# Kernel tuning notes

Hardware: AMD Instinct MI355X
Metric: run time of the kernel (lower is better)

Reference implementation:

```python
import jax, jax.numpy as jnp
import numpy as np
from functools import partial

# --- constants from module init / yolov5 NMS conventions ---
CONF_THRES = 0.25
IOU_THRES = 0.45
PATCH_CONF = 0.001
GN = jnp.array([640.0, 640.0, 640.0, 640.0])  # img_size[[1,0,1,0]]
MAX_WH = 4096.0       # per-class NMS offset trick
K_CLEAN = 256         # fixed-size cap for clean detections (max_det=1000 effectively)
K_PATCH = 1024        # fixed-size cap for patch detections (max_det=30000 effectively)
MAXDET_CLEAN = 1000
MAXDET_PATCH = 30000
B, N, NC = 8, 25200, 80


def xywh2xyxy(x):
    xy, wh = x[..., :2], x[..., 2:4]
    return jnp.concatenate([xy - wh * 0.5, xy + wh * 0.5], axis=-1)


def pairwise_iou(a, b):
    # a: [A,4], b: [B,4] -> [A,B] jaccard overlap (same math as IoU.get_iou)
    tl = jnp.maximum(a[:, None, :2], b[None, :, :2])
    br = jnp.minimum(a[:, None, 2:], b[None, :, 2:])
    wh = jnp.clip(br - tl, 0.0)
    inter = wh[..., 0] * wh[..., 1]
    area_a = (a[:, 2] - a[:, 0]) * (a[:, 3] - a[:, 1])
    area_b = (b[:, 2] - b[:, 0]) * (b[:, 3] - b[:, 1])
    return inter / (area_a[:, None] + area_b[None, :] - inter)


def greedy_nms(iou_mat, valid, iou_thres):
    # iou_mat: [K,K] (score-sorted order), valid: [K] bool. Greedy suppression.
    K = valid.shape[0]
    j = jnp.arange(K)

    def body(i, keep):
        suppress = keep[i] & (iou_mat[i] > iou_thres) & (j > i)
        return keep & ~suppress

    return jax.lax.fori_loop(0, K, body, valid)


def _nms_single(pred, conf_thres, K, max_det):
    # pred: [N, 5+nc] raw yolov5 prediction for one image
    boxes = xywh2xyxy(pred[:, :4])
    obj = pred[:, 4]
    cls_scores = pred[:, 5:] * obj[:, None]          # conf = obj * cls
    conf = cls_scores.max(axis=-1)
    cls = jnp.argmax(cls_scores, axis=-1).astype(pred.dtype)
    valid = (obj > conf_thres) & (conf > conf_thres)
    mscore = jnp.where(valid, conf, -1.0)
    _, idx = jax.lax.top_k(mscore, K)                # fixed-size candidate prefilter
    bk, ck, vk = boxes[idx], cls[idx], valid[idx]
    off_boxes = bk + (ck * MAX_WH)[:, None]          # class-offset NMS
    iou = pairwise_iou(off_boxes, off_boxes)
    keep = greedy_nms(jax.lax.stop_gradient(iou), vk, IOU_THRES)
    keep = keep & (jnp.cumsum(keep.astype(jnp.int32)) <= max_det)
    return bk, ck, keep


def _forward(output_clean, output_patch):
    nms_clean = jax.vmap(lambda p: _nms_single(p, CONF_THRES, K_CLEAN, MAXDET_CLEAN))
    nms_patch = jax.vmap(lambda p: _nms_single(p, PATCH_CONF, K_PATCH, MAXDET_PATCH))
    bc, cc, kc = nms_clean(output_clean)   # [B,Kc,4],[B,Kc],[B,Kc]
    bp, cp, kp = nms_patch(output_patch)   # [B,Kp,4],[B,Kp],[B,Kp]
    bc_n = bc / GN
    bp_n = bp / GN

    def per_img(bp_i, cp_i, kp_i, bc_i, cc_i, kc_i):
        iou = pairwise_iou(bp_i, bc_i)                       # [Kp, Kc]
        match = kp_i[:, None] & (cp_i[:, None] == cc_i[None, :])
        tm = jnp.max(jnp.where(match, iou, 0.0), axis=0)     # max IoU per clean det
        return jnp.sum(jnp.where(kc_i, tm, 0.0)), jnp.sum(kc_i.astype(jnp.float32))

    sums, counts = jax.vmap(per_img)(bp_n, cp, kp, bc_n, cc, kc)
    total, cnt = sums.sum(), counts.sum()
    return jnp.where(cnt > 0, 1.0 - total / jnp.maximum(cnt, 1.0), 1.0)


def setup_inputs() -> dict:
    key = jax.random.key(0)
    k1, k2 = jax.random.split(key)

    def make(k):
        kxy, kwh, ko, kc = jax.random.split(k, 4)
        xy = jax.random.uniform(kxy, (B, N, 2)) * 608.0 + 16.0   # centers in-frame
        wh = jax.random.uniform(kwh, (B, N, 2)) * 96.0 + 8.0     # plausible box sizes
        obj = jax.random.uniform(ko, (B, N, 1))
        cls = jax.random.uniform(kc, (B, N, NC))
        return jnp.concatenate([xy, wh, obj, cls], axis=-1)

    return {"output_clean": make(k1), "output_patch": make(k2)}


def reference(output_clean, output_patch):
    return _forward(output_clean, output_patch)
```

## Files before the change

kernel.cpp:

```cpp
#include <hip/hip_runtime.h>

#define N_ANCH 25200
#define NCLS   80
#define ROW    85
#define NIMG   16
#define KMAX   1024
#define NBINS  1024
#define CAND_CAP 4096
#define SC_ROWS 64
#define SC_CHUNKS 394
#define SC_FLOATS (SC_ROWS*ROW)
#define PCHUNK 64

typedef unsigned long long u64;
typedef unsigned int u32;

#define OFF_KEYS 0ull
#define OFF_HIST 3225600ull
#define OFF_DIAG 3291136ull
#define OFF_SEL  3422208ull
#define OFF_BOX  3553280ull
#define OFF_CLS  3815424ull
#define OFF_RINIT 3880960ull
#define OFF_KEEP 3883008ull
#define WS_NEED  3948544ull
#define ZERO_BYTES 65536ull

#define DMA16(gsrc, ldst) \
    __builtin_amdgcn_global_load_lds( \
        (const __attribute__((address_space(1))) void*)(gsrc), \
        (__attribute__((address_space(3))) void*)(ldst), 16, 0, 0)

__device__ __forceinline__ int key_bin(u64 key) {
    u32 hi = (u32)(key >> 32);
    if (hi == 0u) return 0;
    float conf = __uint_as_float(hi - 0x40000000u);
    int b = 1 + (int)(conf * 1022.0f);
    return b > 1023 ? 1023 : b;
}

__device__ __forceinline__ u64 readlane64(u64 v, int src) {
    u32 lo = (u32)__builtin_amdgcn_readlane((int)(u32)(v & 0xffffffffull), src);
    u32 hi = (u32)__builtin_amdgcn_readlane((int)(u32)(v >> 32), src);
    return ((u64)hi << 32) | (u64)lo;
}

__device__ __forceinline__ u64 shfl64_xor(u64 v, int m) {
    int lo = __shfl_xor((int)(u32)(v & 0xffffffffull), m, 64);
    int hi = __shfl_xor((int)(u32)(v >> 32), m, 64);
    return ((u64)(u32)hi << 32) | (u64)(u32)lo;
}

__global__ __launch_bounds__(128) void k_score(const float* __restrict__ clean,
                                               const float* __restrict__ patch,
                                               u64* __restrict__ keys,
                                               int* __restrict__ hist)
{
    __shared__ float lbuf[SC_FLOATS];
    __shared__ int bh[NBINS];
    const int t = threadIdx.x;
    const int wv = t >> 6, lane = t & 63;
    const int bid = blockIdx.x;
    const int b = bid / SC_CHUNKS;
    const int chunk = bid - b * SC_CHUNKS;
    for (int i = t; i < NBINS; i += 128) bh[i] = 0;
    const float* bufbase = (b < 8) ? clean : patch;
    const float* ibase = bufbase + (size_t)((b < 8) ? b : b - 8) * N_ANCH * ROW;
    const int base = chunk * SC_ROWS;
    const float* g = ibase + (size_t)base * ROW;
    if (chunk != SC_CHUNKS - 1) {
        if (wv == 0) {
            #pragma unroll
            for (int u = 0; u < 11; ++u)
                DMA16(g + u * 256 + lane * 4, lbuf + u * 256);
        } else {
            #pragma unroll
            for (int u = 11; u < 21; ++u)
                DMA16(g + u * 256 + lane * 4, lbuf + u * 256);
            if (lane < 16)
                DMA16(g + 21 * 256 + lane * 4, lbuf + 21 * 256);
        }
    } else {
        const float* lim = bufbase + (size_t)8 * N_ANCH * ROW - 4;
        if (wv == 0) {
            #pragma unroll
            for (int u = 0; u < 11; ++u) {
                const float* s = g + u * 256 + lane * 4;
                if (s > lim) s = lim;
                DMA16(s, lbuf + u * 256);
            }
        } else {
            #pragma unroll
            for (int u = 11; u < 21; ++u) {
                const float* s = g + u * 256 + lane * 4;
                if (s > lim) s = lim;
                DMA16(s, lbuf + u * 256);
            }
            if (lane < 16) {
                const float* s = g + 21 * 256 + lane * 4;
                if (s > lim) s = lim;
                DMA16(s, lbuf + 21 * 256);
            }
        }
    }
    asm volatile("s_waitcnt vmcnt(0)" ::: "memory");
    __syncthreads();
    const int r = t >> 1, h = t & 1;
    const float* p = lbuf + r * ROW;
    const float obj = p[4];
    const int d0 = h * 40;
    float best = -1.0f; int bc = 0;
    #pragma unroll 8
    for (int d = 0; d < 40; ++d) {
        const float s = p[5 + d0 + d] * obj;
        if (s > best) { best = s; bc = d0 + d; }
    }
    const float obest = __shfl_xor(best, 1, 64);
    const int   obc   = __shfl_xor(bc, 1, 64);
    if (h == 0) {
        float fb = best; int fc = bc;
        if (obest > fb) { fb = obest; fc = obc; }
        const int row = base + r;
        if (row < N_ANCH) {
            const float th = (b < 8) ? 0.25f : 0.001f;
            const bool valid = (obj > th) && (fb > th);
            const u32 hi = valid ? (__float_as_uint(fb) + 0x40000000u) : 0u;
            if (valid) {
                int bin = 1 + (int)(fb * 1022.0f);
                if (bin > 1023) bin = 1023;
                atomicAdd(&bh[bin], 1);
            }
            const u32 nbar = 32767u - (u32)row;
            keys[(size_t)b * N_ANCH + row] =
                ((u64)hi << 32) | ((u64)nbar << 8) | (u64)(u32)fc;
        }
    }
    __syncthreads();
    for (int i = t; i < NBINS; i += 128)
        if (bh[i]) atomicAdd(&hist[b * NBINS + i], bh[i]);
}

__global__ __launch_bounds__(1024, 4) void k_tcs(const u64* __restrict__ keys,
                                                 const int* __restrict__ hist,
                                                 u64* __restrict__ sel)
{
    __shared__ u64 sk[CAND_CAP];
    __shared__ int arr[NBINS];
    __shared__ int cnt;
    __shared__ int Tsh;
    const int b = blockIdx.x;
    const int t = threadIdx.x;
    const int K = (b < 8) ? 256 : 1024;
    const u64* kp = keys + (size_t)b * N_ANCH;
    u64 rk[25];
    #pragma unroll
    for (int it = 0; it < 25; ++it) {
        const int i = it * 1024 + t;
        rk[it] = (i < N_ANCH) ? kp[i] : 0ull;
    }
    if (t == 0) cnt = 0;
    const int h = hist[b * NBINS + t];
    arr[t] = h;
    __syncthreads();
    for (int off = 1; off < NBINS; off <<= 1) {
        int v = (t + off < NBINS) ? arr[t + off] : 0;
        __syncthreads();
        arr[t] += v;
        __syncthreads();
    }
    if ((arr[t] - h) < K && arr[t] >= K) Tsh = t;
    __syncthreads();
    const int T = Tsh;
    const int lane = t & 63;
    #pragma unroll
    for (int it = 0; it < 25; ++it) {
        const u64 key = rk[it];
        const bool cnd = (key_bin(key) >= T) && ((it * 1024 + t) < N_ANCH);
        const u64 bal = __ballot(cnd);
        if (bal) {
            int base = 0;
            if (lane == 0) base = atomicAdd(&cnt, __popcll(bal));
            base = __shfl(base, 0, 64);
            if (cnd) {
                const int pos = base + __popcll(bal & ((1ull << lane) - 1ull));
                if (pos < CAND_CAP) sk[pos] = key;
            }
        }
    }
    __syncthreads();
    const int C = min(cnt, CAND_CAP);
    u64 e0, e1, e2, e3;
    e0 = (t < C) ? sk[t] : 0ull;
    e1 = (1024 + t < C) ? sk[1024 + t] : 0ull;
    e2 = (2048 + t < C) ? sk[2048 + t] : 0ull;
    e3 = (3072 + t < C) ? sk[3072 + t] : 0ull;
    __syncthreads();
    #define CSWAP_D(a, c) { if ((a) < (c)) { u64 _t = (a); (a) = (c); (c) = _t; } }
    #define CSWAP_A(a, c) { if ((a) > (c)) { u64 _t = (a); (a) = (c); (c) = _t; } }
    for (int k = 2; k <= 4096; k <<= 1) {
        for (int j = k >> 1; j > 0; j >>= 1) {
            if (j >= 1024) {
                if (j == 2048) { CSWAP_D(e0, e2); CSWAP_D(e1, e3); }
                else {
                    if (k == 4096) { CSWAP_D(e0, e1); CSWAP_D(e2, e3); }
                    else           { CSWAP_D(e0, e1); CSWAP_A(e2, e3); }
                }
            } else if (j >= 64) {
                __syncthreads();
                sk[t] = e0; sk[1024 + t] = e1; sk[2048 + t] = e2; sk[3072 + t] = e3;
                __syncthreads();
                const int tp = t ^ j;
                #pragma unroll
                for (int p = 0; p < 4; ++p) {
                    const int i = p * 1024 + t;
                    const u64 cv = (p == 0) ? e0 : (p == 1) ? e1 : (p == 2) ? e2 : e3;
                    const u64 o = sk[p * 1024 + tp];
                    const bool take_max = (((i & k) == 0) == ((t & j) == 0));
                    const u64 mx = cv > o ? cv : o;
                    const u64 mn = cv > o ? o : cv;
                    const u64 nv = take_max ? mx : mn;
                    if (p == 0) e0 = nv; else if (p == 1) e1 = nv;
                    else if (p == 2) e2 = nv; else e3 = nv;
                }
            } else {
                #pragma unroll
                for (int p = 0; p < 4; ++p) {
                    const int i = p * 1024 + t;
                    const u64 cv = (p == 0) ? e0 : (p == 1) ? e1 : (p == 2) ? e2 : e3;
                    const u64 o = shfl64_xor(cv, j);
                    const bool take_max = (((i & k) == 0) == ((t & j) == 0));
                    const u64 mx = cv > o ? cv : o;
                    const u64 mn = cv > o ? o : cv;
                    const u64 nv = take_max ? mx : mn;
                    if (p == 0) e0 = nv; else if (p == 1) e1 = nv;
                    else if (p == 2) e2 = nv; else e3 = nv;
                }
            }
        }
    }
    if (t < K) sel[b * KMAX + t] = e0;
    #undef CSWAP_D
    #undef CSWAP_A
}

__global__ __launch_bounds__(1024) void k_nms_mask(const float* __restrict__ clean,
                                                   const float* __restrict__ patch,
                                                   const u64* __restrict__ sel,
                                                   float4* __restrict__ boxes,
                                                   int* __restrict__ cls,
                                                   u64* __restrict__ rinit,
                                                   u64* __restrict__ mask,
                                                   u64* __restrict__ diag)
{
    __shared__ float4 bx[KMAX];
    __shared__ float ar[KMAX];
    const int b = blockIdx.x, y = blockIdx.y;
    const int K = (b < 8) ? 256 : 1024;
    const int row0 = y * 64;
    if (row0 >= K) return;
    const int t = threadIdx.x;
    {
        const u64 key = (t < K) ? sel[b * KMAX + t] : 0ull;
        const u32 hi = (u32)(key >> 32);
        const bool valid = (t < K) && (hi != 0u);
        const u64 bal = __ballot(valid);
        if (y == 0 && (t & 63) == 0) rinit[b * 16 + (t >> 6)] = ~bal;
        if (t < K) {
            const int n = 32767 - (int)((key >> 8) & 0x7FFFu);
            const int c = (int)(key & 0x7Fu);
            const float* src = ((b < 8) ? (clean + (size_t)b * N_ANCH * ROW)
                                        : (patch + (size_t)(b - 8) * N_ANCH * ROW))
                               + (size_t)n * ROW;
            const float x = src[0], yy = src[1], w = src[2], h = src[3];
            const float4 raw = make_float4(x - w * 0.5f, yy - h * 0.5f,
                                           x + w * 0.5f, yy + h * 0.5f);
            if (y == 0) { boxes[b * KMAX + t] = raw; cls[b * KMAX + t] = c; }
            const float off = (float)c * 4096.0f;
            const float4 ob = make_float4(raw.x + off, raw.y + off,
                                          raw.z + off, raw.w + off);
            bx[t] = ob;
            ar[t] = (ob.z - ob.x) * (ob.w - ob.y);
        }
    }
    __syncthreads();
    const int w   = t >> 6;
    const int row = row0 + (t & 63);
    u64* dst = mask + ((size_t)b * KMAX + row) * 16 + w;
    if (((w << 6) + 63) <= row0 && row0 > 0) { *dst = 0ull; return; }
    const float4 bi = bx[row];
    const float ai = ar[row];
    const int jbase = w << 6;
    u64 m = 0;
    #pragma unroll 8
    for (int k = 0; k < 64; ++k) {
        const int j = jbase + k;
        const float4 bj = bx[j];
        const float ax = fmaxf(bi.x, bj.x), ay = fmaxf(bi.y, bj.y);
        const float bx2 = fminf(bi.z, bj.z), by2 = fminf(bi.w, bj.w);
        const float iw = fmaxf(bx2 - ax, 0.f), ih = fmaxf(by2 - ay, 0.f);
        const float inter = iw * ih;
        const float iou = inter / (ai + ar[j] - inter);
        if (j > row && iou > 0.45f) m |= (1ull << k);
    }
    *dst = m;
    if (w == (row0 >> 6)) diag[(size_t)b * KMAX + row] = m;
}

__global__ __launch_bounds__(1024) void k_nms_scan(const u64* __restrict__ mask,
                                                   const u64* __restrict__ diag,
                                                   const u64* __restrict__ rinit,
                                                   int* __restrict__ keep)
{
    extern __shared__ u64 smem[];
    const int b = blockIdx.x;
    const int K = (b < 8) ? 256 : 1024;
    const int W = K >> 6;
    const int t = threadIdx.x;
    u64* smask = smem;
    u64* sdiag = smem + (size_t)K * 16;
    {
        const float4* s4 = (const float4*)(mask + (size_t)b * KMAX * 16);
        float4* d4 = (float4*)smask;
        const int n4 = (K * 16) >> 1;
        for (int i = t; i < n4; i += 1024) d4[i] = s4[i];
        const float4* s4d = (const float4*)(diag + (size_t)b * KMAX);
        float4* d4d = (float4*)sdiag;
        for (int i = t; i < (K >> 1); i += 1024) d4d[i] = s4d[i];
    }
    __syncthreads();
    if (t >= 64) return;
    const int lane = t;
    const int q = lane >> 4;
    const int wl = lane & 15;
    u64 w_remv = rinit[b * 16 + wl];
    u64 ow = readlane64(w_remv, 0);
    u64 dj = sdiag[lane];
    for (int g = 0; g < W; ++g) {
        u64 nz = __ballot(dj != 0ull);
        u64 o = ow;
        while (nz) {
            const int j = (int)__builtin_ctzll(nz);
            nz &= nz - 1;
            if (!((o >> j) & 1ull)) o |= readlane64(dj, j);
        }
        const u64 kept = ~o;
        if (g + 1 < W) dj = sdiag[(g + 1) * 64 + lane];
        const u64* mrow = smask + (size_t)(g * 64 + q * 16) * 16 + wl;
        const u32 kg = (u32)((kept >> (q * 16)) & 0xFFFFull);
        u64 a0 = 0, a1 = 0;
        #pragma unroll
        for (int i = 0; i < 16; i += 2) {
            const u64 m0 = mrow[(size_t)(i + 0) * 16];
            const u64 m1 = mrow[(size_t)(i + 1) * 16];
            a0 |= ((kg >> i) & 1u) ? m0 : 0ull;
            a1 |= ((kg >> (i + 1)) & 1u) ? m1 : 0ull;
        }
        u64 part = a0 | a1;
        part |= shfl64_xor(part, 16);
        part |= shfl64_xor(part, 32);
        w_remv |= part;
        if (g + 1 < W) ow = readlane64(w_remv, g + 1);
    }
    if (lane < W) {
        #pragma unroll
        for (int k = 0; k < 64; ++k)
            keep[b * KMAX + lane * 64 + k] = (int)(((w_remv >> k) & 1) ^ 1ull);
    }
}

__global__ __launch_bounds__(256) void k_match_partial(const float4* __restrict__ boxes,
                                                       const int* __restrict__ cls,
                                                       const int* __restrict__ keep,
                                                       float* __restrict__ pmax)
{
    __shared__ float4 pb[PCHUNK];
    __shared__ float par[PCHUNK];
    __shared__ int pcls[PCHUNK];
    const int c = blockIdx.x;
    const int p = blockIdx.y;
    const int bp = 8 + c;
    const int t = threadIdx.x;
    if (t < PCHUNK) {
        const int i = p * PCHUNK + t;
        const float4 v = boxes[bp * KMAX + i];
        pb[t] = v;
        par[t] = (v.z - v.x) * (v.w - v.y);
        pcls[t] = keep[bp * KMAX + i] ? cls[bp * KMAX + i] : -1;
    }
    __syncthreads();
    const float4 bc = boxes[c * KMAX + t];
    const int cc = cls[c * KMAX + t];
    const float area_c = (bc.z - bc.x) * (bc.w - bc.y);
    float tm = 0.f;
    #pragma unroll 8
    for (int i = 0; i < PCHUNK; ++i) {
        const float4 bi = pb[i];
        const float ax = fmaxf(bi.x, bc.x), ay = fmaxf(bi.y, bc.y);
        const float bx2 = fminf(bi.z, bc.z), by2 = fminf(bi.w, bc.w);
        const float iw = fmaxf(bx2 - ax, 0.f), ih = fmaxf(by2 - ay, 0.f);
        const float inter = iw * ih;
        const float iou = inter / (par[i] + area_c - inter);
        tm = fmaxf(tm, (pcls[i] == cc) ? iou : 0.f);
    }
    pmax[(c * 16 + p) * 256 + t] = tm;
}

__global__ __launch_bounds__(256) void k_match_final(const float* __restrict__ pmax,
                                                     const int* __restrict__ keep,
                                                     float* __restrict__ out)
{
    __shared__ float red[8];
    const int t = threadIdx.x;
    float tot = 0.f, cn = 0.f;
    for (int c = 0; c < 8; ++c) {
        float tm = 0.f;
        #pragma unroll
        for (int p = 0; p < 16; ++p)
            tm = fmaxf(tm, pmax[(c * 16 + p) * 256 + t]);
        const int kc = keep[c * KMAX + t];
        float val = kc ? tm : 0.f;
        float cv  = kc ? 1.f : 0.f;
        for (int off = 32; off > 0; off >>= 1) {
            val += __shfl_down(val, off);
            cv  += __shfl_down(cv, off);
        }
        const int wv = t >> 6, lane = t & 63;
        if (lane == 0) { red[wv] = val; red[4 + wv] = cv; }
        __syncthreads();
        if (t == 0) {
            tot += red[0] + red[1] + red[2] + red[3];
            cn  += red[4] + red[5] + red[6] + red[7];
        }
        __syncthreads();
    }
    if (t == 0)
        out[0] = (cn > 0.f) ? (1.0f - tot / fmaxf(cn, 1.0f)) : 1.0f;
}

extern "C" void kernel_launch(void* const* d_in, const int* in_sizes, int n_in,
                              void* d_out, int out_size, void* d_ws, size_t ws_size,
                              hipStream_t stream)
{
    if (ws_size < WS_NEED) return;
    const float* clean = (const float*)d_in[0];
    const float* patch = (const float*)d_in[1];
    float* out = (float*)d_out;
    char* ws = (char*)d_ws;

    u64*    keys = (u64*)(ws + OFF_KEYS);
    u64*    mask = (u64*)(ws + OFF_KEYS);
    int*    hist = (int*)(ws + OFF_HIST);
    u64*    diag = (u64*)(ws + OFF_DIAG);
    float*  pmax = (float*)(ws + OFF_DIAG);
    u64*    sel  = (u64*)(ws + OFF_SEL);
    float4* boxes = (float4*)(ws + OFF_BOX);
    int*    cls  = (int*)(ws + OFF_CLS);
    u64*    rinit = (u64*)(ws + OFF_RINIT);
    int*    keep = (int*)(ws + OFF_KEEP);

    hipMemsetAsync(ws + OFF_HIST, 0, ZERO_BYTES, stream);

    k_score<<<NIMG * SC_CHUNKS, 128, 0, stream>>>(clean, patch, keys, hist);
    k_tcs<<<NIMG, 1024, 0, stream>>>(keys, hist, sel);
    k_nms_mask<<<dim3(NIMG, 16), 1024, 0, stream>>>(clean, patch, sel, boxes, cls,
                                                    rinit, mask, diag);
    k_nms_scan<<<NIMG, 1024, KMAX * 16 * 8 + KMAX * 8, stream>>>(mask, diag, rinit, keep);
    k_match_partial<<<dim3(8, 16), 256, 0, stream>>>(boxes, cls, keep, pmax);
    k_match_final<<<1, 256, 0, stream>>>(pmax, keep, out);
}
```

Before: 135.2 us.

## Split threshold-compaction from bitonic sort into separate multi-block kernels

The single per-image kernel that loaded all 25200 keys, found the histogram threshold and compacted the candidates is split in two. Compaction now runs across 16 blocks per image, using a global atomic counter and writing candidates to workspace. A separate kernel then does the bitonic sort from that buffer. The goal is to spread the key scan over many more CUs, at the cost of an extra launch, global atomics and a round trip through global memory.

```diff
diff --git a/kernel.cpp b/kernel.cpp
--- a/kernel.cpp
+++ b/kernel.cpp
@@ -11,20 +11,22 @@
 #define SC_CHUNKS 394
 #define SC_FLOATS (SC_ROWS*ROW)
 #define PCHUNK 64
+#define CCNT_STRIDE 16
 
 typedef unsigned long long u64;
 typedef unsigned int u32;
 
 #define OFF_KEYS 0ull
 #define OFF_HIST 3225600ull
-#define OFF_DIAG 3291136ull
-#define OFF_SEL  3422208ull
-#define OFF_BOX  3553280ull
-#define OFF_CLS  3815424ull
-#define OFF_RINIT 3880960ull
-#define OFF_KEEP 3883008ull
-#define WS_NEED  3948544ull
-#define ZERO_BYTES 65536ull
+#define OFF_CCNT 3291136ull
+#define OFF_CAND 3292160ull
+#define OFF_SEL  3816448ull
+#define OFF_BOX  3947520ull
+#define OFF_CLS  4209664ull
+#define OFF_RINIT 4275200ull
+#define OFF_KEEP 4277248ull
+#define WS_NEED  4342784ull
+#define ZERO_BYTES 66560ull
 
 #define DMA16(gsrc, ldst) \
     __builtin_amdgcn_global_load_lds( \
@@ -140,61 +142,73 @@
         if (bh[i]) atomicAdd(&hist[b * NBINS + i], bh[i]);
 }
 
-__global__ __launch_bounds__(1024, 4) void k_tcs(const u64* __restrict__ keys,
+__global__ __launch_bounds__(256) void k_compact(const u64* __restrict__ keys,
                                                  const int* __restrict__ hist,
-                                                 u64* __restrict__ sel)
-{
-    __shared__ u64 sk[CAND_CAP];
-    __shared__ int arr[NBINS];
-    __shared__ int cnt;
+                                                 int* __restrict__ ccnt,
+                                                 u64* __restrict__ cand)
+{
+    __shared__ int arr[256];
     __shared__ int Tsh;
     const int b = blockIdx.x;
     const int t = threadIdx.x;
     const int K = (b < 8) ? 256 : 1024;
-    const u64* kp = keys + (size_t)b * N_ANCH;
-    u64 rk[25];
-    #pragma unroll
-    for (int it = 0; it < 25; ++it) {
-        const int i = it * 1024 + t;
-        rk[it] = (i < N_ANCH) ? kp[i] : 0ull;
-    }
-    if (t == 0) cnt = 0;
-    const int h = hist[b * NBINS + t];
-    arr[t] = h;
-    __syncthreads();
-    for (int off = 1; off < NBINS; off <<= 1) {
-        int v = (t + off < NBINS) ? arr[t + off] : 0;
+    int hh[4];
+    hh[0] = hist[b * NBINS + 4 * t + 0];
+    hh[1] = hist[b * NBINS + 4 * t + 1];
+    hh[2] = hist[b * NBINS + 4 * t + 2];
+    hh[3] = hist[b * NBINS + 4 * t + 3];
+    const int r = hh[0] + hh[1] + hh[2] + hh[3];
+    arr[t] = r;
+    __syncthreads();
+    for (int off = 1; off < 256; off <<= 1) {
+        int v = (t + off < 256) ? arr[t + off] : 0;
         __syncthreads();
         arr[t] += v;
         __syncthreads();
     }
-    if ((arr[t] - h) < K && arr[t] >= K) Tsh = t;
+    int cb = arr[t] - r;
+    for (int d = 3; d >= 0; --d) {
+        int ca = cb + hh[d];
+        if (cb < K && ca >= K) Tsh = 4 * t + d;
+        cb = ca;
+    }
     __syncthreads();
     const int T = Tsh;
+    const u64* kp = keys + (size_t)b * N_ANCH;
+    const int start = blockIdx.y * 1575;
     const int lane = t & 63;
     #pragma unroll
-    for (int it = 0; it < 25; ++it) {
-        const u64 key = rk[it];
-        const bool cnd = (key_bin(key) >= T) && ((it * 1024 + t) < N_ANCH);
+    for (int it = 0; it < 7; ++it) {
+        const int off = it * 256 + t;
+        const bool in = off < 1575;
+        const u64 key = in ? kp[start + off] : 0ull;
+        const bool cnd = in && (key_bin(key) >= T);
         const u64 bal = __ballot(cnd);
         if (bal) {
             int base = 0;
-            if (lane == 0) base = atomicAdd(&cnt, __popcll(bal));
+            if (lane == 0) base = atomicAdd(&ccnt[b * CCNT_STRIDE], __popcll(bal));
             base = __shfl(base, 0, 64);
             if (cnd) {
                 const int pos = base + __popcll(bal & ((1ull << lane) - 1ull));
-                if (pos < CAND_CAP) sk[pos] = key;
-            }
-        }
-    }
-    __syncthreads();
-    const int C = min(cnt, CAND_CAP);
+                if (pos < CAND_CAP) cand[(size_t)b * CAND_CAP + pos] = key;
+            }
+        }
+    }
+}
+
+__global__ __launch_bounds__(1024) void k_sort(const u64* __restrict__ cand,
+                                               const int* __restrict__ ccnt,
+                                               u64* __restrict__ sel)
+{
+    __shared__ u64 sk[CAND_CAP];
+    const int b = blockIdx.x;
+    const int C = min(ccnt[b * CCNT_STRIDE], CAND_CAP);
+    const int t = threadIdx.x;
     u64 e0, e1, e2, e3;
-    e0 = (t < C) ? sk[t] : 0ull;
-    e1 = (1024 + t < C) ? sk[1024 + t] : 0ull;
-    e2 = (2048 + t < C) ? sk[2048 + t] : 0ull;
-    e3 = (3072 + t < C) ? sk[3072 + t] : 0ull;
-    __syncthreads();
+    e0 = (t < C) ? cand[(size_t)b * CAND_CAP + t] : 0ull;
+    e1 = (1024 + t < C) ? cand[(size_t)b * CAND_CAP + 1024 + t] : 0ull;
+    e2 = (2048 + t < C) ? cand[(size_t)b * CAND_CAP + 2048 + t] : 0ull;
+    e3 = (3072 + t < C) ? cand[(size_t)b * CAND_CAP + 3072 + t] : 0ull;
     #define CSWAP_D(a, c) { if ((a) < (c)) { u64 _t = (a); (a) = (c); (c) = _t; } }
     #define CSWAP_A(a, c) { if ((a) > (c)) { u64 _t = (a); (a) = (c); (c) = _t; } }
     for (int k = 2; k <= 4096; k <<= 1) {
@@ -238,6 +252,7 @@
             }
         }
     }
+    const int K = (b < 8) ? 256 : 1024;
     if (t < K) sel[b * KMAX + t] = e0;
     #undef CSWAP_D
     #undef CSWAP_A
@@ -450,8 +465,10 @@
     u64*    keys = (u64*)(ws + OFF_KEYS);
     u64*    mask = (u64*)(ws + OFF_KEYS);
     int*    hist = (int*)(ws + OFF_HIST);
-    u64*    diag = (u64*)(ws + OFF_DIAG);
-    float*  pmax = (float*)(ws + OFF_DIAG);
+    int*    ccnt = (int*)(ws + OFF_CCNT);
+    u64*    cand = (u64*)(ws + OFF_CAND);
+    u64*    diag = (u64*)(ws + OFF_CAND);
+    float*  pmax = (float*)(ws + OFF_CAND);
     u64*    sel  = (u64*)(ws + OFF_SEL);
     float4* boxes = (float4*)(ws + OFF_BOX);
     int*    cls  = (int*)(ws + OFF_CLS);
@@ -461,7 +478,8 @@
     hipMemsetAsync(ws + OFF_HIST, 0, ZERO_BYTES, stream);
 
     k_score<<<NIMG * SC_CHUNKS, 128, 0, stream>>>(clean, patch, keys, hist);
-    k_tcs<<<NIMG, 1024, 0, stream>>>(keys, hist, sel);
+    k_compact<<<dim3(NIMG, 16), 256, 0, stream>>>(keys, hist, ccnt, cand);
+    k_sort<<<NIMG, 1024, 0, stream>>>(cand, ccnt, sel);
     k_nms_mask<<<dim3(NIMG, 16), 1024, 0, stream>>>(clean, patch, sel, boxes, cls,
                                                     rinit, mask, diag);
     k_nms_scan<<<NIMG, 1024, KMAX * 16 * 8 + KMAX * 8, stream>>>(mask, diag, rinit, keep);
```

New measurement: 137.2 us. About the same (+1.5%).
